# Performance work log

Measured on AMD Instinct MI355X. Metric: run time of the kernel, lower is better.

Reference implementation:

```python
import jax, jax.numpy as jnp
import numpy as np

B = 32768      # batch
N_IN = 128     # input nodes
L = 8          # topological layers
W = 256        # nodes per layer
K = 16         # fan-in per node


def setup_inputs() -> dict:
    key = jax.random.key(0)
    k_x, k_w, k_b, k_e = jax.random.split(key, 4)
    inputs = jax.random.normal(k_x, (B, N_IN), dtype=jnp.float32)
    # scale weights down so sigmoid isn't saturated with fan-in 16
    weights = jax.random.normal(k_w, (L, W, K), dtype=jnp.float32) * 0.25
    biases = jax.random.normal(k_b, (L, W), dtype=jnp.float32) * 0.1
    # DAG-valid edges: layer l may only gather from the N_IN + l*W already-computed nodes
    ek = jax.random.split(k_e, L)
    edge_idx = jnp.stack([
        jax.random.randint(ek[l], (W, K), 0, N_IN + l * W, dtype=jnp.int32)
        for l in range(L)
    ])  # [L, W, K]
    return {"inputs": inputs, "weights": weights, "biases": biases,
            "edge_idx": edge_idx}


def reference(inputs, weights, biases, edge_idx):
    # values buffer starts as the input-node activations: [B, N_IN]
    vals = inputs
    n_layers = weights.shape[0]
    for l in range(n_layers):
        gathered = vals[:, edge_idx[l]]                      # [B, W, K] per-node gather
        pre = jnp.einsum('bwk,wk->bw', gathered, weights[l]) + biases[l]
        vals = jnp.concatenate([vals, jax.nn.sigmoid(pre)], axis=1)
    # output nodes are the last layer, concatenated in order
    return vals[:, -W:]
```

## Files before the change

kernel.cpp:

```cpp
#include <hip/hip_runtime.h>
#include <hip/hip_bf16.h>
#include <hip/hip_fp16.h>


#define NB   32768
#define NIN  128
#define NL   8
#define NW   256
#define NK   16
#define RPB  8
#define STORED (NIN + (NL - 1) * NW)
#define NPARAM (NL * NW * NK)

typedef __fp16 fp16v2 __attribute__((ext_vector_type(2)));

__device__ __forceinline__ unsigned pk16(float a, float b) {
    fp16v2 p = __builtin_amdgcn_cvt_pkrtz(a, b);
    return __builtin_bit_cast(unsigned, p);
}

__device__ __forceinline__ __half2 as_h2(unsigned u) {
    return __builtin_bit_cast(__half2, u);
}

__device__ __forceinline__ void fma_feat(__half2 acc[4], __half2 w2, uint4 p) {
    acc[0] = __hfma2(as_h2(p.x), w2, acc[0]);
    acc[1] = __hfma2(as_h2(p.y), w2, acc[1]);
    acc[2] = __hfma2(as_h2(p.z), w2, acc[2]);
    acc[3] = __hfma2(as_h2(p.w), w2, acc[3]);
}

template <bool PRE>
__global__ __launch_bounds__(256, 5)
void ffn_gather_kernel(const float* __restrict__ inputs,
                       const float* __restrict__ weights,
                       const float* __restrict__ biases,
                       const int*   __restrict__ edge_idx,
                       const int*   __restrict__ idxb,
                       const unsigned* __restrict__ wpk,
                       float* __restrict__ out)
{
    __shared__ uint4 vals[STORED];

    const int t = threadIdx.x;
    const long long row0 = (long long)blockIdx.x * RPB;
    const char* vbase = (const char*)vals;

    if (t < NIN) {
        float v[RPB];
        #pragma unroll
        for (int r = 0; r < RPB; ++r) v[r] = inputs[(row0 + r) * NIN + t];
        uint4 p;
        p.x = pk16(v[0], v[1]);
        p.y = pk16(v[2], v[3]);
        p.z = pk16(v[4], v[5]);
        p.w = pk16(v[6], v[7]);
        vals[t] = p;
    }
    __syncthreads();

    #pragma unroll
    for (int l = 0; l < NL; ++l) {
        const int base = (l * NW + t) * NK;

        const float b = biases[l * NW + t];
        __half2 acc[4];
        const __half2 bb = __float2half2_rn(b);
        #pragma unroll
        for (int j = 0; j < 4; ++j) acc[j] = bb;

        #pragma unroll
        for (int kk = 0; kk < NK / 4; ++kk) {
            int4 o4;
            __half2 w0, w1, w2, w3;
            if (PRE) {
                o4 = ((const int4*)(idxb + base))[kk];
                uint4 wp = ((const uint4*)(wpk + base))[kk];
                w0 = as_h2(wp.x); w1 = as_h2(wp.y);
                w2 = as_h2(wp.z); w3 = as_h2(wp.w);
            } else {
                int4 i4 = ((const int4*)(edge_idx + base))[kk];
                o4.x = i4.x << 4; o4.y = i4.y << 4;
                o4.z = i4.z << 4; o4.w = i4.w << 4;
                float4 w4 = ((const float4*)(weights + base))[kk];
                w0 = __float2half2_rn(w4.x);
                w1 = __float2half2_rn(w4.y);
                w2 = __float2half2_rn(w4.z);
                w3 = __float2half2_rn(w4.w);
            }
            const uint4 p0 = *(const uint4*)(vbase + o4.x);
            const uint4 p1 = *(const uint4*)(vbase + o4.y);
            const uint4 p2 = *(const uint4*)(vbase + o4.z);
            const uint4 p3 = *(const uint4*)(vbase + o4.w);
            fma_feat(acc, w0, p0);
            fma_feat(acc, w1, p1);
            fma_feat(acc, w2, p2);
            fma_feat(acc, w3, p3);
        }

        float s[RPB];
        #pragma unroll
        for (int j = 0; j < 4; ++j) {
            s[2 * j + 0] = 1.0f / (1.0f + __expf(-__low2float(acc[j])));
            s[2 * j + 1] = 1.0f / (1.0f + __expf(-__high2float(acc[j])));
        }

        if (l < NL - 1) {
            uint4 p;
            p.x = pk16(s[0], s[1]);
            p.y = pk16(s[2], s[3]);
            p.z = pk16(s[4], s[5]);
            p.w = pk16(s[6], s[7]);
            vals[NIN + l * NW + t] = p;
            __syncthreads();
        } else {
            #pragma unroll
            for (int r = 0; r < RPB; ++r)
                out[(row0 + r) * NW + t] = s[r];
        }
    }
}

__global__ __launch_bounds__(256)
void prepass_kernel(const float* __restrict__ weights,
                    const int* __restrict__ edge_idx,
                    int* __restrict__ idxb,
                    unsigned* __restrict__ wpk)
{
    const int i = blockIdx.x * 256 + threadIdx.x;
    idxb[i] = edge_idx[i] << 4;
    const float w = weights[i];
    wpk[i] = pk16(w, w);
}

extern "C" void kernel_launch(void* const* d_in, const int* in_sizes, int n_in,
                              void* d_out, int out_size, void* d_ws, size_t ws_size,
                              hipStream_t stream)
{
    const float* inputs   = (const float*)d_in[0];
    const float* weights  = (const float*)d_in[1];
    const float* biases   = (const float*)d_in[2];
    const int*   edge_idx = (const int*)d_in[3];
    float* out = (float*)d_out;

    dim3 grid(NB / RPB);
    dim3 block(NW);

    const size_t need = (size_t)NPARAM * 4 * 2;
    if (ws_size >= need) {
        int*      idxb = (int*)d_ws;
        unsigned* wpk  = (unsigned*)((char*)d_ws + (size_t)NPARAM * 4);
        prepass_kernel<<<NPARAM / 256, 256, 0, stream>>>(weights, edge_idx,
                                                         idxb, wpk);
        ffn_gather_kernel<true><<<grid, block, 0, stream>>>(
            inputs, weights, biases, edge_idx, idxb, wpk, out);
    } else {
        ffn_gather_kernel<false><<<grid, block, 0, stream>>>(
            inputs, weights, biases, edge_idx, nullptr, nullptr, out);
    }
}
```

Before: 139.2 us.

## Reorder per-node edges to spread LDS banks and use fast reciprocal sigmoid

The prepass now sorts each node's 16 edges by the low 3 bits of the source index and rotates the order by a lane-dependent phase. The aim is that lanes of a wave hit different LDS banks when they gather 16-byte node values, which cuts bank conflicts. The sigmoid now uses the hardware approximate reciprocal instead of a full division. The cost is a serial per-thread insertion sort in a smaller prepass launch, plus slightly less accurate sigmoid outputs.

```diff
diff --git a/kernel.cpp b/kernel.cpp
--- a/kernel.cpp
+++ b/kernel.cpp
@@ -21,6 +21,10 @@
 
 __device__ __forceinline__ __half2 as_h2(unsigned u) {
     return __builtin_bit_cast(__half2, u);
+}
+
+__device__ __forceinline__ float fast_sigmoid(float x) {
+    return __builtin_amdgcn_rcpf(1.0f + __expf(-x));
 }
 
 __device__ __forceinline__ void fma_feat(__half2 acc[4], __half2 w2, uint4 p) {
@@ -101,8 +105,8 @@
         float s[RPB];
         #pragma unroll
         for (int j = 0; j < 4; ++j) {
-            s[2 * j + 0] = 1.0f / (1.0f + __expf(-__low2float(acc[j])));
-            s[2 * j + 1] = 1.0f / (1.0f + __expf(-__high2float(acc[j])));
+            s[2 * j + 0] = fast_sigmoid(__low2float(acc[j]));
+            s[2 * j + 1] = fast_sigmoid(__high2float(acc[j]));
         }
 
         if (l < NL - 1) {
@@ -127,10 +131,32 @@
                     int* __restrict__ idxb,
                     unsigned* __restrict__ wpk)
 {
-    const int i = blockIdx.x * 256 + threadIdx.x;
-    idxb[i] = edge_idx[i] << 4;
-    const float w = weights[i];
-    wpk[i] = pk16(w, w);
+    const int u = blockIdx.x * 256 + threadIdx.x;
+    if (u >= NL * NW) return;
+    const int base = u * NK;
+
+    int   idx[NK];
+    float w[NK];
+    for (int k = 0; k < NK; ++k) {
+        idx[k] = edge_idx[base + k];
+        w[k]   = weights[base + k];
+    }
+    for (int i = 1; i < NK; ++i) {
+        const int vi = idx[i]; const float vw = w[i];
+        const int gi = vi & 7;
+        int j = i - 1;
+        while (j >= 0 && (idx[j] & 7) > gi) {
+            idx[j + 1] = idx[j]; w[j + 1] = w[j]; --j;
+        }
+        idx[j + 1] = vi; w[j + 1] = vw;
+    }
+    const int lane  = u & 63;
+    const int phase = ((lane & 7) << 1) | ((lane >> 3) & 1);
+    for (int s = 0; s < NK; ++s) {
+        const int k = (s + phase) & (NK - 1);
+        idxb[base + s] = idx[k] << 4;
+        wpk[base + s]  = pk16(w[k], w[k]);
+    }
 }
 
 extern "C" void kernel_launch(void* const* d_in, const int* in_sizes, int n_in,
@@ -150,8 +176,8 @@
     if (ws_size >= need) {
         int*      idxb = (int*)d_ws;
         unsigned* wpk  = (unsigned*)((char*)d_ws + (size_t)NPARAM * 4);
-        prepass_kernel<<<NPARAM / 256, 256, 0, stream>>>(weights, edge_idx,
-                                                         idxb, wpk);
+        prepass_kernel<<<(NL * NW + 255) / 256, 256, 0, stream>>>(
+            weights, edge_idx, idxb, wpk);
         ffn_gather_kernel<true><<<grid, block, 0, stream>>>(
             inputs, weights, biases, edge_idx, idxb, wpk, out);
     } else {
```

Measured after the change: 161.4 us. 16.0% more time.

## Reorder per-node fan-in edges to balance LDS banks; use rcp sigmoid

Applied to the files above, without the earlier changes.

The prepass now reorders each node's 16 edges so that, at every gather step, the 64 lanes of a wavefront spread their 16-byte LDS reads across the 8 bank groups (idx mod 8), using ballots to count collisions and greedily re-picking edges. The goal is to cut LDS bank conflicts in the gather-heavy main kernel. The sigmoid also switches from a true division to a hardware reciprocal approximation. The trade-off is a serial prepass on only 8 blocks, which adds latency before the main kernel, and slightly lower sigmoid accuracy.

```diff
diff --git a/kernel.cpp b/kernel.cpp
--- a/kernel.cpp
+++ b/kernel.cpp
@@ -21,6 +21,10 @@
 
 __device__ __forceinline__ __half2 as_h2(unsigned u) {
     return __builtin_bit_cast(__half2, u);
+}
+
+__device__ __forceinline__ float fast_sigmoid(float x) {
+    return __builtin_amdgcn_rcpf(1.0f + __expf(-x));
 }
 
 __device__ __forceinline__ void fma_feat(__half2 acc[4], __half2 w2, uint4 p) {
@@ -101,8 +105,8 @@
         float s[RPB];
         #pragma unroll
         for (int j = 0; j < 4; ++j) {
-            s[2 * j + 0] = 1.0f / (1.0f + __expf(-__low2float(acc[j])));
-            s[2 * j + 1] = 1.0f / (1.0f + __expf(-__high2float(acc[j])));
+            s[2 * j + 0] = fast_sigmoid(__low2float(acc[j]));
+            s[2 * j + 1] = fast_sigmoid(__high2float(acc[j]));
         }
 
         if (l < NL - 1) {
@@ -127,10 +131,62 @@
                     int* __restrict__ idxb,
                     unsigned* __restrict__ wpk)
 {
-    const int i = blockIdx.x * 256 + threadIdx.x;
-    idxb[i] = edge_idx[i] << 4;
-    const float w = weights[i];
-    wpk[i] = pk16(w, w);
+    __shared__ int   p_idx[4][64][NK];
+    __shared__ float p_w[4][64][NK];
+
+    const int wid  = threadIdx.x >> 6;
+    const int lane = threadIdx.x & 63;
+    const int prob = blockIdx.x * 4 + wid;
+    const int l    = prob >> 2;
+    const int wv   = prob & 3;
+    const int base = (l * NW + wv * 64 + lane) * NK;
+
+    unsigned long long gpack = 0;
+    for (int k = 0; k < NK; ++k) {
+        const int idx = edge_idx[base + k];
+        p_idx[wid][lane][k] = idx;
+        p_w[wid][lane][k]   = weights[base + k];
+        gpack |= (unsigned long long)(idx & 7) << (4 * k);
+    }
+    __syncthreads();
+
+    const unsigned long long lt = (lane == 0) ? 0ull
+                                : (~0ull >> (64 - lane));
+    unsigned rem = 0xFFFFu;
+
+    for (int s = 0; s < NK; ++s) {
+        int prop_k = __ffs(rem) - 1;
+        int prop_g = (int)((gpack >> (4 * prop_k)) & 7);
+
+        for (int iter = 0; iter < 3; ++iter) {
+            unsigned long long cntpack = 0;
+            int myrank = 0;
+            #pragma unroll
+            for (int g = 0; g < 8; ++g) {
+                const unsigned long long m = __ballot(prop_g == g);
+                cntpack |= (unsigned long long)__popcll(m) << (8 * g);
+                if (prop_g == g) myrank = (int)__popcll(m & lt);
+            }
+            if (myrank >= 8) {
+                int bestc = 1 << 20, bk = prop_k, bg = prop_g;
+                #pragma unroll
+                for (int kk = 0; kk < NK; ++kk) {
+                    const int k = (kk + lane * 3) & (NK - 1);
+                    if (rem & (1u << k)) {
+                        const int g = (int)((gpack >> (4 * k)) & 7);
+                        const int c = (int)((cntpack >> (8 * g)) & 0xff);
+                        if (c < bestc) { bestc = c; bk = k; bg = g; }
+                    }
+                }
+                prop_k = bk; prop_g = bg;
+            }
+        }
+
+        rem &= ~(1u << prop_k);
+        const float w = p_w[wid][lane][prop_k];
+        idxb[base + s] = p_idx[wid][lane][prop_k] << 4;
+        wpk[base + s]  = pk16(w, w);
+    }
 }
 
 extern "C" void kernel_launch(void* const* d_in, const int* in_sizes, int n_in,
@@ -150,8 +206,7 @@
     if (ws_size >= need) {
         int*      idxb = (int*)d_ws;
         unsigned* wpk  = (unsigned*)((char*)d_ws + (size_t)NPARAM * 4);
-        prepass_kernel<<<NPARAM / 256, 256, 0, stream>>>(weights, edge_idx,
-                                                         idxb, wpk);
+        prepass_kernel<<<8, 256, 0, stream>>>(weights, edge_idx, idxb, wpk);
         ffn_gather_kernel<true><<<grid, block, 0, stream>>>(
             inputs, weights, biases, edge_idx, idxb, wpk, out);
     } else {
```

After: 173.9 us. 1.25x slower.

## Reorder per-node edges to spread LDS bank groups across lanes in prepass

Applied to the files above, without the earlier changes.

The prepass now permutes each node's K edges so that, at each k-step, groups of 8 adjacent threads read from different LDS bank groups (index mod 8), using greedy per-octet scheduling by group degree. This aims to reduce LDS bank conflicts on the 16-byte gathers in the main kernel. The sigmoid also switches to a hardware reciprocal approximation. The prepass becomes a serial 4-block, 64-thread kernel, which adds launch latency that could offset the gains.

```diff
diff --git a/kernel.cpp b/kernel.cpp
--- a/kernel.cpp
+++ b/kernel.cpp
@@ -21,6 +21,10 @@
 
 __device__ __forceinline__ __half2 as_h2(unsigned u) {
     return __builtin_bit_cast(__half2, u);
+}
+
+__device__ __forceinline__ float fast_sigmoid(float x) {
+    return __builtin_amdgcn_rcpf(1.0f + __expf(-x));
 }
 
 __device__ __forceinline__ void fma_feat(__half2 acc[4], __half2 w2, uint4 p) {
@@ -101,8 +105,8 @@
         float s[RPB];
         #pragma unroll
         for (int j = 0; j < 4; ++j) {
-            s[2 * j + 0] = 1.0f / (1.0f + __expf(-__low2float(acc[j])));
-            s[2 * j + 1] = 1.0f / (1.0f + __expf(-__high2float(acc[j])));
+            s[2 * j + 0] = fast_sigmoid(__low2float(acc[j]));
+            s[2 * j + 1] = fast_sigmoid(__high2float(acc[j]));
         }
 
         if (l < NL - 1) {
@@ -121,16 +125,79 @@
     }
 }
 
-__global__ __launch_bounds__(256)
+__global__ __launch_bounds__(64)
 void prepass_kernel(const float* __restrict__ weights,
                     const int* __restrict__ edge_idx,
                     int* __restrict__ idxb,
                     unsigned* __restrict__ wpk)
 {
-    const int i = blockIdx.x * 256 + threadIdx.x;
-    idxb[i] = edge_idx[i] << 4;
-    const float w = weights[i];
-    wpk[i] = pk16(w, w);
+    __shared__ unsigned long long ws_cnt[64][8];
+    __shared__ unsigned long long ws_st[64][8];
+    __shared__ unsigned long long ws_sorted[64][8];
+
+    const int t    = threadIdx.x;
+    const int prob = blockIdx.x * 64 + t;
+    const int l    = prob >> 5;
+    const int oct  = prob & 31;
+    const int u0   = l * NW + oct * 8;
+
+    unsigned long long deg = 0;
+    for (int lane = 0; lane < 8; ++lane) {
+        const int base = (u0 + lane) * NK;
+        unsigned long long gp = 0, cnt = 0;
+        for (int k = 0; k < NK; ++k) {
+            const int g = edge_idx[base + k] & 7;
+            gp  |= (unsigned long long)g << (4 * k);
+            cnt += 1ull << (8 * g);
+        }
+        unsigned long long st = 0; unsigned acc = 0;
+        for (int g = 0; g < 8; ++g) {
+            st  |= (unsigned long long)acc << (8 * g);
+            acc += (unsigned)((cnt >> (8 * g)) & 0xff);
+        }
+        unsigned long long sorted = 0, fill = st;
+        for (int k = 0; k < NK; ++k) {
+            const int g   = (int)((gp >> (4 * k)) & 7);
+            const int pos = (int)((fill >> (8 * g)) & 0xff);
+            sorted |= (unsigned long long)k << (4 * pos);
+            fill   += 1ull << (8 * g);
+        }
+        ws_cnt[t][lane]    = cnt;
+        ws_st[t][lane]     = st;
+        ws_sorted[t][lane] = sorted;
+        deg += cnt;
+    }
+
+    for (int s = 0; s < NK; ++s) {
+        unsigned used = 0;
+        for (int lane = 0; lane < 8; ++lane) {
+            const unsigned long long cnt = ws_cnt[t][lane];
+            int bg = -1, bd = -1, fg = -1, fd = -1;
+            #pragma unroll
+            for (int g = 0; g < 8; ++g) {
+                const int c = (int)((cnt >> (8 * g)) & 0xff);
+                if (c) {
+                    const int d = (int)((deg >> (8 * g)) & 0xff);
+                    if (d > fd) { fd = d; fg = g; }
+                    if (!((used >> g) & 1) && d > bd) { bd = d; bg = g; }
+                }
+            }
+            const int g = (bg >= 0) ? bg : fg;
+            const unsigned long long st = ws_st[t][lane];
+            const int pos = (int)((st >> (8 * g)) & 0xff);
+            const int k   = (int)((ws_sorted[t][lane] >> (4 * pos)) & 0xf);
+            ws_st[t][lane]  = st + (1ull << (8 * g));
+            ws_cnt[t][lane] = cnt - (1ull << (8 * g));
+            deg  -= 1ull << (8 * g);
+            used |= 1u << g;
+
+            const int src = (u0 + lane) * NK + k;
+            const int dst = (u0 + lane) * NK + s;
+            idxb[dst] = edge_idx[src] << 4;
+            const float w = weights[src];
+            wpk[dst] = pk16(w, w);
+        }
+    }
 }
 
 extern "C" void kernel_launch(void* const* d_in, const int* in_sizes, int n_in,
@@ -150,8 +217,7 @@
     if (ws_size >= need) {
         int*      idxb = (int*)d_ws;
         unsigned* wpk  = (unsigned*)((char*)d_ws + (size_t)NPARAM * 4);
-        prepass_kernel<<<NPARAM / 256, 256, 0, stream>>>(weights, edge_idx,
-                                                         idxb, wpk);
+        prepass_kernel<<<4, 64, 0, stream>>>(weights, edge_idx, idxb, wpk);
         ffn_gather_kernel<true><<<grid, block, 0, stream>>>(
             inputs, weights, biases, edge_idx, idxb, wpk, out);
     } else {
```

Result: slower. 199.6 us (+43.4%).
